# Kernel tuning notes

Measured on AMD Instinct MI355X. Metric: run time of the kernel, lower is better.

Reference implementation:

```python
import jax, jax.numpy as jnp
import numpy as np

N = 100000       # n_entities + n_users
E = 1000000      # edges
D = 64           # entity_dim (phase/mod half-width)
R = 40           # n_relations
PI = 3.1415926235897933
GAMMA = 12.0
EMB_RANGE = (GAMMA + 2.0) / D   # (gamma + epsilon) / entity_dim
DIMS = [128, 64, 32, 16]        # conv_dim_list = [2*D] + [64,32,16]


def setup_inputs() -> dict:
    key = jax.random.key(0)
    ks = jax.random.split(key, 20)
    inp = {}
    inp["entity_embed"] = jax.random.uniform(ks[0], (N, 2 * D), minval=-EMB_RANGE, maxval=EMB_RANGE, dtype=jnp.float32)
    inp["rel_embed"] = jax.random.uniform(ks[1], (R, 3 * D), minval=-EMB_RANGE, maxval=EMB_RANGE, dtype=jnp.float32)
    inp["phase_w"] = jnp.array([[0.5 * EMB_RANGE]], dtype=jnp.float32)
    inp["mod_w"] = jnp.array([[1.0]], dtype=jnp.float32)
    names = [("W1_0", "b1_0", "W2_0", "b2_0"), ("W1_1", "b1_1", "W2_1", "b2_1"), ("W1_2", "b1_2", "W1_2b", "b2_2")]
    for i, (w1n, b1n, w2n, b2n) in enumerate(names):
        din, dout = DIMS[i], DIMS[i + 1]
        s = 1.0 / np.sqrt(din)
        inp[w1n] = jax.random.uniform(ks[2 + 4 * i], (dout, din), minval=-s, maxval=s, dtype=jnp.float32)
        inp[b1n] = jax.random.uniform(ks[3 + 4 * i], (dout,), minval=-s, maxval=s, dtype=jnp.float32)
        inp[w2n] = jax.random.uniform(ks[4 + 4 * i], (dout, din), minval=-s, maxval=s, dtype=jnp.float32)
        inp[b2n] = jax.random.uniform(ks[5 + 4 * i], (dout,), minval=-s, maxval=s, dtype=jnp.float32)
    inp["src"] = jax.random.randint(ks[14], (E,), 0, N, dtype=jnp.int32)
    inp["dst"] = jax.random.randint(ks[15], (E,), 0, N, dtype=jnp.int32)
    inp["etype"] = jax.random.randint(ks[16], (E,), 0, R, dtype=jnp.int32)
    return inp


def _edge_att(entity_embed, rel_embed, phase_w, mod_w, src, dst, etype):
    # HAKE att_score: h = dst node, t = src node (per original code)
    h = entity_embed[dst]            # [E, 2D]
    t = entity_embed[src]            # [E, 2D]
    r = rel_embed[etype]             # [E, 3D]
    scale = EMB_RANGE / PI
    ph, mh = h[:, :D], h[:, D:]
    pr, mr, br = r[:, :D], r[:, D:2 * D], r[:, 2 * D:]
    pt, mt = t[:, :D], t[:, D:]
    mr = jnp.abs(mr)
    br = jnp.minimum(br, 1.0)
    br = jnp.where(br < -mr, -mr, br)  # conditional write bias_relation[indicator] = -mod_relation
    mod_score = jnp.linalg.norm(mh * (mr + br) - mt * (1.0 - br), axis=1) * mod_w[0, 0]
    phase = (ph + pr - pt) / scale
    phase_score = jnp.sum(jnp.abs(jnp.sin(phase / 2.0)), axis=1) * phase_w[0, 0]
    att = phase_score + mod_score    # [E]
    # edge softmax over incoming edges of each dst node
    amax = jax.ops.segment_max(att, dst, num_segments=N)
    ex = jnp.exp(att - amax[dst])
    den = jax.ops.segment_sum(ex, dst, num_segments=N)
    return ex / den[dst]


def reference(entity_embed, rel_embed, phase_w, mod_w,
              W1_0, b1_0, W2_0, b2_0,
              W1_1, b1_1, W2_1, b2_1,
              W1_2, b1_2, W1_2b, b2_2,
              src, dst, etype):
    att = _edge_att(entity_embed, rel_embed, phase_w, mod_w, src, dst, etype)

    def layer(node, W1, b1, W2, b2):
        # u_mul_e('node','att','side') + sum('side','N_h')
        msg = node[src] * att[:, None]                    # [E, din]
        Nh = jax.ops.segment_sum(msg, dst, num_segments=N)
        # bi-interaction aggregator
        o = jax.nn.leaky_relu((node + Nh) @ W1.T + b1) + jax.nn.leaky_relu((node * Nh) @ W2.T + b2)
        nrm = jnp.linalg.norm(o, axis=1, keepdims=True)
        return o, o / jnp.maximum(nrm, 1e-12)             # (ego_embed, F.normalize)

    ego = entity_embed
    outs = [ego]
    for (W1, b1, W2, b2) in [(W1_0, b1_0, W2_0, b2_0), (W1_1, b1_1, W2_1, b2_1), (W1_2, b1_2, W1_2b, b2_2)]:
        ego, normed = layer(ego, W1, b1, W2, b2)
        outs.append(normed)
    return jnp.concatenate(outs, axis=1)                   # [N, 128+64+32+16]
```

## Files before the change

kernel.cpp:

```cpp
#include <hip/hip_runtime.h>
#include <math.h>


__global__ void hist_kernel(const int* __restrict__ dst, int* __restrict__ cnt,
                            int nedges) {
    int e = blockIdx.x * blockDim.x + threadIdx.x;
    if (e < nedges) atomicAdd(&cnt[dst[e]], 1);
}

__global__ __launch_bounds__(1024) void scan_block_kernel(
    const int* __restrict__ cnt, int* __restrict__ rowptr,
    int* __restrict__ bsum, int n) {
    __shared__ int swv[16];
    int tid = threadIdx.x, lane = tid & 63, wid = tid >> 6;
    int i = blockIdx.x * 1024 + tid;
    int v = (i < n) ? cnt[i] : 0;
    #pragma unroll
    for (int off = 1; off < 64; off <<= 1) {
        int t = __shfl_up(v, off, 64);
        if (lane >= off) v += t;
    }
    if (lane == 63) swv[wid] = v;
    __syncthreads();
    if (wid == 0) {
        int s = (lane < 16) ? swv[lane] : 0;
        #pragma unroll
        for (int off = 1; off < 16; off <<= 1) {
            int t = __shfl_up(s, off, 64);
            if (lane >= off) s += t;
        }
        if (lane < 16) swv[lane] = s;
    }
    __syncthreads();
    int offv = wid ? swv[wid - 1] : 0;
    if (i < n) rowptr[i + 1] = v + offv;
    if (tid == 1023) bsum[blockIdx.x] = v + offv;
}

__global__ __launch_bounds__(64) void scan_tops_kernel(
    const int* __restrict__ bsum, int* __restrict__ boff, int nb) {
    int l = threadIdx.x;
    int a = (2 * l < nb) ? bsum[2 * l] : 0;
    int b = (2 * l + 1 < nb) ? bsum[2 * l + 1] : 0;
    int s = a + b;
    #pragma unroll
    for (int off = 1; off < 64; off <<= 1) {
        int t = __shfl_up(s, off, 64);
        if (l >= off) s += t;
    }
    int excl = s - (a + b);
    if (2 * l < nb) boff[2 * l] = excl;
    if (2 * l + 1 < nb) boff[2 * l + 1] = excl + a;
}

__global__ __launch_bounds__(1024) void scan_add_kernel(
    int* __restrict__ rowptr, const int* __restrict__ boff, int n) {
    int i = blockIdx.x * 1024 + threadIdx.x;
    if (i < n) rowptr[i + 1] += boff[blockIdx.x];
    if (i == 0) rowptr[0] = 0;
}

__global__ void fill_kernel(const int* __restrict__ src, const int* __restrict__ dst,
                            const int* __restrict__ etype,
                            const int* __restrict__ rowptr, int* __restrict__ cursor,
                            int* __restrict__ se_s, int nedges) {
    int e = blockIdx.x * blockDim.x + threadIdx.x;
    if (e >= nedges) return;
    int d = dst[e];
    int slot = rowptr[d] + atomicAdd(&cursor[d], 1);
    se_s[slot] = src[e] | (etype[e] << 17);
}

__global__ void rel_prep_kernel(const float* __restrict__ rel,
                                float* __restrict__ relp, int nrel) {
    int i = blockIdx.x * blockDim.x + threadIdx.x;
    if (i >= nrel * 64) return;
    int r = i >> 6, d = i & 63;
    float pr = rel[r * 192 + d];
    float mr = fabsf(rel[r * 192 + 64 + d]);
    float br = rel[r * 192 + 128 + d];
    br = fminf(br, 1.0f);
    br = fmaxf(br, -mr);
    relp[r * 192 + d]       = mr + br;
    relp[r * 192 + 64 + d]  = 1.0f - br;
    relp[r * 192 + 128 + d] = pr;
}

__global__ __launch_bounds__(256) void att_gather_kernel(
    const float* __restrict__ embed, const float* __restrict__ relp,
    const float* __restrict__ pw, const float* __restrict__ mw,
    const int* __restrict__ se_s, const int* __restrict__ rowptr,
    float* __restrict__ att_s, float* __restrict__ ai,
    float* __restrict__ Nh, int nnodes)
{
    int v = blockIdx.x * 4 + (threadIdx.x >> 6);
    if (v >= nnodes) return;
    int lane = threadIdx.x & 63;
    int sub = lane >> 5;
    int c = lane & 31;
    int beg = rowptr[v];
    int deg = rowptr[v + 1] - beg;

    const float K = (float)(0.5 * 3.1415926235897933 / 0.21875);
    float mwv = mw[0], pwv = pw[0];

    float4 h4 = *(const float4*)(embed + (size_t)v * 128 + 4 * c);

    float den = 0.0f;
    float4 acc = make_float4(0.f, 0.f, 0.f, 0.f);

    #pragma unroll 2
    for (int k0 = 0; k0 < deg; k0 += 2) {
        int ke = k0 + sub;
        bool valid = ke < deg;
        int kc = beg + (valid ? ke : 0);
        int se = se_s[kc];
        int sidx = se & 0x1FFFF;
        int r = se >> 17;
        float4 t4 = *(const float4*)(embed + (size_t)sidx * 128 + 4 * c);
        float rv;
        if (c < 16) {
            float4 P4 = *(const float4*)(relp + r * 192 + 128 + 4 * c);
            rv  = fabsf(__sinf((h4.x + P4.x - t4.x) * K));
            rv += fabsf(__sinf((h4.y + P4.y - t4.y) * K));
            rv += fabsf(__sinf((h4.z + P4.z - t4.z) * K));
            rv += fabsf(__sinf((h4.w + P4.w - t4.w) * K));
        } else {
            float4 A4 = *(const float4*)(relp + r * 192 + 4 * (c - 16));
            float4 B4 = *(const float4*)(relp + r * 192 + 64 + 4 * (c - 16));
            float d0 = h4.x * A4.x - t4.x * B4.x;
            float d1 = h4.y * A4.y - t4.y * B4.y;
            float d2 = h4.z * A4.z - t4.z * B4.z;
            float d3 = h4.w * A4.w - t4.w * B4.w;
            rv = (d0 * d0 + d1 * d1) + (d2 * d2 + d3 * d3);
        }
        #pragma unroll
        for (int off = 1; off < 16; off <<= 1)
            rv += __shfl_xor(rv, off, 64);
        float other = __shfl_xor(rv, 16, 64);
        float ppv = (c < 16) ? rv : other;
        float qqv = (c < 16) ? other : rv;
        float s = sqrtf(qqv) * mwv + ppv * pwv;
        float w = valid ? __expf(s) : 0.0f;
        den += w;
        acc.x = fmaf(w, t4.x, acc.x);
        acc.y = fmaf(w, t4.y, acc.y);
        acc.z = fmaf(w, t4.z, acc.z);
        acc.w = fmaf(w, t4.w, acc.w);
        if (valid && c == 0) att_s[kc] = w;
    }
    acc.x += __shfl_xor(acc.x, 32, 64);
    acc.y += __shfl_xor(acc.y, 32, 64);
    acc.z += __shfl_xor(acc.z, 32, 64);
    acc.w += __shfl_xor(acc.w, 32, 64);
    den += __shfl_xor(den, 32, 64);
    float invd = (deg > 0) ? 1.0f / den : 0.0f;
    if (sub == 0) {
        float4 o = make_float4(acc.x * invd, acc.y * invd,
                               acc.z * invd, acc.w * invd);
        *(float4*)(Nh + (size_t)v * 128 + 4 * c) = o;
        if (c == 0) ai[v] = invd;
    }
}

template<int DIN>
__global__ __launch_bounds__(256) void gather_kernel(
    const float* __restrict__ node, int nstride, const float* __restrict__ nrm,
    const float* __restrict__ att_s, const int* __restrict__ se_s,
    const int* __restrict__ rowptr, const float* __restrict__ ai,
    float* __restrict__ Nh, int nnodes)
{
    constexpr int LPE = DIN / 4;
    constexpr int EP  = 64 / LPE;
    constexpr int U   = 4;
    int v = blockIdx.x * 4 + (threadIdx.x >> 6);
    if (v >= nnodes) return;
    int lane = threadIdx.x & 63;
    int sub = lane / LPE;
    int c = lane % LPE;
    int beg = rowptr[v];
    int deg = rowptr[v + 1] - beg;

    float4 acc = make_float4(0.f, 0.f, 0.f, 0.f);
    for (int kb = 0; kb < deg; kb += 64) {
        int kc = kb + lane;
        bool inr = kc < deg;
        int sv = inr ? (se_s[beg + kc] & 0x1FFFF) : 0;
        float av = inr ? att_s[beg + kc] * nrm[sv] : 0.0f;
        int kmax = min(64, deg - kb);
        for (int k0 = 0; k0 < kmax; k0 += U * EP) {
            float a[U];
            const float4* p[U];
            #pragma unroll
            for (int u = 0; u < U; ++u) {
                int kk = k0 + u * EP + sub;
                bool val = kk < kmax;
                int kidx = val ? kk : 0;
                int ssrc = __shfl(sv, kidx, 64);
                float aa = __shfl(av, kidx, 64);
                a[u] = val ? aa : 0.0f;
                p[u] = (const float4*)(node + (size_t)ssrc * nstride + 4 * c);
            }
            float4 rv[U];
            #pragma unroll
            for (int u = 0; u < U; ++u) rv[u] = *p[u];
            #pragma unroll
            for (int u = 0; u < U; ++u) {
                acc.x += a[u] * rv[u].x;
                acc.y += a[u] * rv[u].y;
                acc.z += a[u] * rv[u].z;
                acc.w += a[u] * rv[u].w;
            }
        }
    }
    #pragma unroll
    for (int off = LPE; off < 64; off <<= 1) {
        acc.x += __shfl_xor(acc.x, off, 64);
        acc.y += __shfl_xor(acc.y, off, 64);
        acc.z += __shfl_xor(acc.z, off, 64);
        acc.w += __shfl_xor(acc.w, off, 64);
    }
    if (sub == 0) {
        float aiv = ai[v];
        float4 o = make_float4(acc.x * aiv, acc.y * aiv,
                               acc.z * aiv, acc.w * aiv);
        *(float4*)(Nh + (size_t)v * DIN + 4 * c) = o;
    }
}

template<int DIN, int DOUT, bool NRM>
__global__ __launch_bounds__(512) void gemm_kernel(
    const float* __restrict__ node, int nstride, const float* __restrict__ nrm_in,
    const float* __restrict__ Nh,
    const float* __restrict__ W1, const float* __restrict__ b1,
    const float* __restrict__ W2, const float* __restrict__ b2,
    float* __restrict__ out, int out_col, float* __restrict__ nrm_out, int nnodes)
{
    constexpr int XS = DIN + 1;
    constexpr int DH = DOUT / 8;
    __shared__ float sx1[64 * XS], sx2[64 * XS];
    __shared__ float sred[8][64];

    int tid = threadIdx.x;
    int tile0 = blockIdx.x * 64;

    for (int idx = tid; idx < 64 * (DIN / 4); idx += 512) {
        int row = idx / (DIN / 4), c = idx % (DIN / 4);
        int v = tile0 + row;
        float4 nv4 = make_float4(0.f, 0.f, 0.f, 0.f);
        float4 hv4 = make_float4(0.f, 0.f, 0.f, 0.f);
        if (v < nnodes) {
            nv4 = *(const float4*)(node + (size_t)v * nstride + 4 * c);
            hv4 = *(const float4*)(Nh + (size_t)v * DIN + 4 * c);
            if (NRM) {
                float rn = nrm_in[v];
                nv4.x *= rn; nv4.y *= rn; nv4.z *= rn; nv4.w *= rn;
            }
        }
        float* p1 = sx1 + row * XS + 4 * c;
        float* p2 = sx2 + row * XS + 4 * c;
        p1[0] = nv4.x + hv4.x; p1[1] = nv4.y + hv4.y;
        p1[2] = nv4.z + hv4.z; p1[3] = nv4.w + hv4.w;
        p2[0] = nv4.x * hv4.x; p2[1] = nv4.y * hv4.y;
        p2[2] = nv4.z * hv4.z; p2[3] = nv4.w * hv4.w;
    }
    __syncthreads();

    int lane = tid & 63;
    int jh = __builtin_amdgcn_readfirstlane(tid >> 6);
    int j0 = jh * DH;
    int v = tile0 + lane;
    bool act = v < nnodes;

    float acc1[DH], acc2[DH];
    #pragma unroll
    for (int j = 0; j < DH; ++j) { acc1[j] = 0.f; acc2[j] = 0.f; }

    const float* px1 = sx1 + lane * XS;
    const float* px2 = sx2 + lane * XS;
    #pragma unroll 1
    for (int ic = 0; ic < DIN; ic += 8) {
        float x1c[8], x2c[8];
        #pragma unroll
        for (int t = 0; t < 8; ++t) {
            x1c[t] = px1[ic + t];
            x2c[t] = px2[ic + t];
        }
        #pragma unroll
        for (int j = 0; j < DH; ++j) {
            const float* w1 = W1 + (size_t)(j0 + j) * DIN + ic;
            const float* w2 = W2 + (size_t)(j0 + j) * DIN + ic;
            #pragma unroll
            for (int t = 0; t < 8; ++t) {
                acc1[j] = fmaf(x1c[t], w1[t], acc1[j]);
                acc2[j] = fmaf(x2c[t], w2[t], acc2[j]);
            }
        }
    }

    float o[DH];
    float ss = 0.0f;
    #pragma unroll
    for (int j = 0; j < DH; ++j) {
        float a1 = acc1[j] + b1[j0 + j];
        a1 = a1 >= 0.0f ? a1 : 0.01f * a1;
        float a2 = acc2[j] + b2[j0 + j];
        a2 = a2 >= 0.0f ? a2 : 0.01f * a2;
        o[j] = a1 + a2;
        ss += o[j] * o[j];
    }
    sred[jh][lane] = ss;
    __syncthreads();
    float tot = 0.0f;
    #pragma unroll
    for (int q = 0; q < 8; ++q) tot += sred[q][lane];
    float nv2 = fmaxf(sqrtf(tot), 1e-12f);
    float inv = 1.0f / nv2;
    if (act) {
        float* po = out + (size_t)v * 240 + out_col + j0;
        if (DH >= 4) {
            #pragma unroll
            for (int j = 0; j < DH; j += 4) {
                float4 st = make_float4(o[j] * inv, o[j + 1] * inv,
                                        o[j + 2] * inv, o[j + 3] * inv);
                *(float4*)(po + j) = st;
            }
        } else {
            #pragma unroll
            for (int j = 0; j < DH; ++j) po[j] = o[j] * inv;
        }
        if (nrm_out && jh == 0) nrm_out[v] = nv2;
    }
}

__global__ void copy_ego_kernel(const float* __restrict__ embed,
                                float* __restrict__ out, int nnodes) {
    int tid = blockIdx.x * blockDim.x + threadIdx.x;
    if (tid >= nnodes * 32) return;
    int v = tid >> 5;
    int c = tid & 31;
    float4 val = *(const float4*)(embed + (size_t)v * 128 + 4 * c);
    *(float4*)(out + (size_t)v * 240 + 4 * c) = val;
}

extern "C" void kernel_launch(void* const* d_in, const int* in_sizes, int n_in,
                              void* d_out, int out_size, void* d_ws, size_t ws_size,
                              hipStream_t stream) {
    const float* embed = (const float*)d_in[0];
    const float* rel   = (const float*)d_in[1];
    const float* pw    = (const float*)d_in[2];
    const float* mw    = (const float*)d_in[3];
    const float* W1_0  = (const float*)d_in[4];
    const float* b1_0  = (const float*)d_in[5];
    const float* W2_0  = (const float*)d_in[6];
    const float* b2_0  = (const float*)d_in[7];
    const float* W1_1  = (const float*)d_in[8];
    const float* b1_1  = (const float*)d_in[9];
    const float* W2_1  = (const float*)d_in[10];
    const float* b2_1  = (const float*)d_in[11];
    const float* W1_2  = (const float*)d_in[12];
    const float* b1_2  = (const float*)d_in[13];
    const float* W1_2b = (const float*)d_in[14];
    const float* b2_2  = (const float*)d_in[15];
    const int* src   = (const int*)d_in[16];
    const int* dst   = (const int*)d_in[17];
    const int* etype = (const int*)d_in[18];
    float* out = (float*)d_out;

    const int n = in_sizes[0] / 128;
    const int e = in_sizes[16];
    const int r = in_sizes[1] / 192;

    char* ws = (char*)d_ws;
    float* att_s  = (float*)ws;
    int*   se_s   = (int*)(att_s + e);
    float* Nh     = (float*)(se_s + e);
    int*   rowptr = (int*)(Nh + (size_t)n * 128);
    int*   cnt    = rowptr + n + 1;
    int*   cursor = cnt + n;
    int*   bsum   = cursor + n;
    int*   boff   = bsum + 128;
    float* nrm1   = (float*)(boff + 128);
    float* nrm2   = nrm1 + n;
    float* relp   = nrm2 + n;
    float* ai     = relp + r * 192;

    const int NB = (n + 1023) / 1024;

    hipMemsetAsync(cnt, 0, (size_t)(2 * n) * 4, stream);
    hist_kernel<<<(e + 255) / 256, 256, 0, stream>>>(dst, cnt, e);
    scan_block_kernel<<<NB, 1024, 0, stream>>>(cnt, rowptr, bsum, n);
    scan_tops_kernel<<<1, 64, 0, stream>>>(bsum, boff, NB);
    scan_add_kernel<<<NB, 1024, 0, stream>>>(rowptr, boff, n);
    fill_kernel<<<(e + 255) / 256, 256, 0, stream>>>(src, dst, etype, rowptr,
                                                     cursor, se_s, e);
    rel_prep_kernel<<<(r * 64 + 255) / 256, 256, 0, stream>>>(rel, relp, r);

    int gblocks = (n + 3) / 4;
    int tiles = (n + 63) / 64;

    att_gather_kernel<<<gblocks, 256, 0, stream>>>(
        embed, relp, pw, mw, se_s, rowptr, att_s, ai, Nh, n);

    gemm_kernel<128, 64, false><<<tiles, 512, 0, stream>>>(
        embed, 128, nullptr, Nh, W1_0, b1_0, W2_0, b2_0, out, 128, nrm1, n);
    gather_kernel<64><<<gblocks, 256, 0, stream>>>(
        out + 128, 240, nrm1, att_s, se_s, rowptr, ai, Nh, n);
    gemm_kernel<64, 32, true><<<tiles, 512, 0, stream>>>(
        out + 128, 240, nrm1, Nh, W1_1, b1_1, W2_1, b2_1, out, 192, nrm2, n);
    gather_kernel<32><<<gblocks, 256, 0, stream>>>(
        out + 192, 240, nrm2, att_s, se_s, rowptr, ai, Nh, n);
    gemm_kernel<32, 16, true><<<tiles, 512, 0, stream>>>(
        out + 192, 240, nrm2, Nh, W1_2, b1_2, W1_2b, b2_2, out, 224, nullptr, n);

    copy_ego_kernel<<<(n * 32 + 255) / 256, 256, 0, stream>>>(embed, out, n);
}
```

Baseline: 517.8 us.

## Process eight edges per wavefront in attention gather and fuse ego copy into GEMM

The attention gather kernel now maps 8 lanes to each edge, each lane covering 8 phase and 8 modulus elements, so one wavefront handles 8 edges per iteration instead of 2. This cuts the shuffle-reduction depth per edge and improves memory-level parallelism for low-degree nodes, at the cost of more registers per lane and a longer final cross-group reduction. Separately, the first-layer GEMM writes the ego embedding into the output while it loads its tile, which removes the standalone copy kernel and its extra read of the embedding.

```diff
diff --git a/kernel.cpp b/kernel.cpp
--- a/kernel.cpp
+++ b/kernel.cpp
@@ -96,70 +96,110 @@
     int v = blockIdx.x * 4 + (threadIdx.x >> 6);
     if (v >= nnodes) return;
     int lane = threadIdx.x & 63;
-    int sub = lane >> 5;
-    int c = lane & 31;
+    int g = lane >> 3;
+    int q = lane & 7;
     int beg = rowptr[v];
     int deg = rowptr[v + 1] - beg;
 
     const float K = (float)(0.5 * 3.1415926235897933 / 0.21875);
     float mwv = mw[0], pwv = pw[0];
 
-    float4 h4 = *(const float4*)(embed + (size_t)v * 128 + 4 * c);
+    const float* hrow = embed + (size_t)v * 128;
+    float4 hp0 = *(const float4*)(hrow + 8 * q);
+    float4 hp1 = *(const float4*)(hrow + 8 * q + 4);
+    float4 hm0 = *(const float4*)(hrow + 64 + 8 * q);
+    float4 hm1 = *(const float4*)(hrow + 64 + 8 * q + 4);
 
     float den = 0.0f;
-    float4 acc = make_float4(0.f, 0.f, 0.f, 0.f);
-
-    #pragma unroll 2
-    for (int k0 = 0; k0 < deg; k0 += 2) {
-        int ke = k0 + sub;
+    float4 ap0 = make_float4(0.f, 0.f, 0.f, 0.f);
+    float4 ap1 = make_float4(0.f, 0.f, 0.f, 0.f);
+    float4 am0 = make_float4(0.f, 0.f, 0.f, 0.f);
+    float4 am1 = make_float4(0.f, 0.f, 0.f, 0.f);
+
+    for (int k0 = 0; k0 < deg; k0 += 8) {
+        int ke = k0 + g;
         bool valid = ke < deg;
         int kc = beg + (valid ? ke : 0);
         int se = se_s[kc];
         int sidx = se & 0x1FFFF;
         int r = se >> 17;
-        float4 t4 = *(const float4*)(embed + (size_t)sidx * 128 + 4 * c);
-        float rv;
-        if (c < 16) {
-            float4 P4 = *(const float4*)(relp + r * 192 + 128 + 4 * c);
-            rv  = fabsf(__sinf((h4.x + P4.x - t4.x) * K));
-            rv += fabsf(__sinf((h4.y + P4.y - t4.y) * K));
-            rv += fabsf(__sinf((h4.z + P4.z - t4.z) * K));
-            rv += fabsf(__sinf((h4.w + P4.w - t4.w) * K));
-        } else {
-            float4 A4 = *(const float4*)(relp + r * 192 + 4 * (c - 16));
-            float4 B4 = *(const float4*)(relp + r * 192 + 64 + 4 * (c - 16));
-            float d0 = h4.x * A4.x - t4.x * B4.x;
-            float d1 = h4.y * A4.y - t4.y * B4.y;
-            float d2 = h4.z * A4.z - t4.z * B4.z;
-            float d3 = h4.w * A4.w - t4.w * B4.w;
-            rv = (d0 * d0 + d1 * d1) + (d2 * d2 + d3 * d3);
-        }
+        const float* trow = embed + (size_t)sidx * 128;
+        float4 tp0 = *(const float4*)(trow + 8 * q);
+        float4 tp1 = *(const float4*)(trow + 8 * q + 4);
+        float4 tm0 = *(const float4*)(trow + 64 + 8 * q);
+        float4 tm1 = *(const float4*)(trow + 64 + 8 * q + 4);
+        const float* rrow = relp + r * 192;
+        float4 A0 = *(const float4*)(rrow + 8 * q);
+        float4 A1 = *(const float4*)(rrow + 8 * q + 4);
+        float4 B0 = *(const float4*)(rrow + 64 + 8 * q);
+        float4 B1 = *(const float4*)(rrow + 64 + 8 * q + 4);
+        float4 P0 = *(const float4*)(rrow + 128 + 8 * q);
+        float4 P1 = *(const float4*)(rrow + 128 + 8 * q + 4);
+
+        float pp;
+        pp  = fabsf(__sinf((hp0.x + P0.x - tp0.x) * K));
+        pp += fabsf(__sinf((hp0.y + P0.y - tp0.y) * K));
+        pp += fabsf(__sinf((hp0.z + P0.z - tp0.z) * K));
+        pp += fabsf(__sinf((hp0.w + P0.w - tp0.w) * K));
+        pp += fabsf(__sinf((hp1.x + P1.x - tp1.x) * K));
+        pp += fabsf(__sinf((hp1.y + P1.y - tp1.y) * K));
+        pp += fabsf(__sinf((hp1.z + P1.z - tp1.z) * K));
+        pp += fabsf(__sinf((hp1.w + P1.w - tp1.w) * K));
+
+        float d0 = hm0.x * A0.x - tm0.x * B0.x;
+        float d1 = hm0.y * A0.y - tm0.y * B0.y;
+        float d2 = hm0.z * A0.z - tm0.z * B0.z;
+        float d3 = hm0.w * A0.w - tm0.w * B0.w;
+        float d4 = hm1.x * A1.x - tm1.x * B1.x;
+        float d5 = hm1.y * A1.y - tm1.y * B1.y;
+        float d6 = hm1.z * A1.z - tm1.z * B1.z;
+        float d7 = hm1.w * A1.w - tm1.w * B1.w;
+        float qq = ((d0 * d0 + d1 * d1) + (d2 * d2 + d3 * d3)) +
+                   ((d4 * d4 + d5 * d5) + (d6 * d6 + d7 * d7));
+
         #pragma unroll
-        for (int off = 1; off < 16; off <<= 1)
-            rv += __shfl_xor(rv, off, 64);
-        float other = __shfl_xor(rv, 16, 64);
-        float ppv = (c < 16) ? rv : other;
-        float qqv = (c < 16) ? other : rv;
-        float s = sqrtf(qqv) * mwv + ppv * pwv;
+        for (int off = 1; off < 8; off <<= 1) {
+            pp += __shfl_xor(pp, off, 64);
+            qq += __shfl_xor(qq, off, 64);
+        }
+        float s = sqrtf(qq) * mwv + pp * pwv;
         float w = valid ? __expf(s) : 0.0f;
         den += w;
-        acc.x = fmaf(w, t4.x, acc.x);
-        acc.y = fmaf(w, t4.y, acc.y);
-        acc.z = fmaf(w, t4.z, acc.z);
-        acc.w = fmaf(w, t4.w, acc.w);
-        if (valid && c == 0) att_s[kc] = w;
-    }
-    acc.x += __shfl_xor(acc.x, 32, 64);
-    acc.y += __shfl_xor(acc.y, 32, 64);
-    acc.z += __shfl_xor(acc.z, 32, 64);
-    acc.w += __shfl_xor(acc.w, 32, 64);
-    den += __shfl_xor(den, 32, 64);
+        ap0.x = fmaf(w, tp0.x, ap0.x); ap0.y = fmaf(w, tp0.y, ap0.y);
+        ap0.z = fmaf(w, tp0.z, ap0.z); ap0.w = fmaf(w, tp0.w, ap0.w);
+        ap1.x = fmaf(w, tp1.x, ap1.x); ap1.y = fmaf(w, tp1.y, ap1.y);
+        ap1.z = fmaf(w, tp1.z, ap1.z); ap1.w = fmaf(w, tp1.w, ap1.w);
+        am0.x = fmaf(w, tm0.x, am0.x); am0.y = fmaf(w, tm0.y, am0.y);
+        am0.z = fmaf(w, tm0.z, am0.z); am0.w = fmaf(w, tm0.w, am0.w);
+        am1.x = fmaf(w, tm1.x, am1.x); am1.y = fmaf(w, tm1.y, am1.y);
+        am1.z = fmaf(w, tm1.z, am1.z); am1.w = fmaf(w, tm1.w, am1.w);
+        if (valid && q == 0) att_s[kc] = w;
+    }
+
+    #pragma unroll
+    for (int off = 8; off < 64; off <<= 1) {
+        ap0.x += __shfl_xor(ap0.x, off, 64); ap0.y += __shfl_xor(ap0.y, off, 64);
+        ap0.z += __shfl_xor(ap0.z, off, 64); ap0.w += __shfl_xor(ap0.w, off, 64);
+        ap1.x += __shfl_xor(ap1.x, off, 64); ap1.y += __shfl_xor(ap1.y, off, 64);
+        ap1.z += __shfl_xor(ap1.z, off, 64); ap1.w += __shfl_xor(ap1.w, off, 64);
+        am0.x += __shfl_xor(am0.x, off, 64); am0.y += __shfl_xor(am0.y, off, 64);
+        am0.z += __shfl_xor(am0.z, off, 64); am0.w += __shfl_xor(am0.w, off, 64);
+        am1.x += __shfl_xor(am1.x, off, 64); am1.y += __shfl_xor(am1.y, off, 64);
+        am1.z += __shfl_xor(am1.z, off, 64); am1.w += __shfl_xor(am1.w, off, 64);
+        den += __shfl_xor(den, off, 64);
+    }
     float invd = (deg > 0) ? 1.0f / den : 0.0f;
-    if (sub == 0) {
-        float4 o = make_float4(acc.x * invd, acc.y * invd,
-                               acc.z * invd, acc.w * invd);
-        *(float4*)(Nh + (size_t)v * 128 + 4 * c) = o;
-        if (c == 0) ai[v] = invd;
+    if (g == 0) {
+        float* pn = Nh + (size_t)v * 128;
+        *(float4*)(pn + 8 * q) = make_float4(ap0.x * invd, ap0.y * invd,
+                                             ap0.z * invd, ap0.w * invd);
+        *(float4*)(pn + 8 * q + 4) = make_float4(ap1.x * invd, ap1.y * invd,
+                                                 ap1.z * invd, ap1.w * invd);
+        *(float4*)(pn + 64 + 8 * q) = make_float4(am0.x * invd, am0.y * invd,
+                                                  am0.z * invd, am0.w * invd);
+        *(float4*)(pn + 64 + 8 * q + 4) = make_float4(am1.x * invd, am1.y * invd,
+                                                      am1.z * invd, am1.w * invd);
+        if (q == 0) ai[v] = invd;
     }
 }
 
@@ -228,7 +268,7 @@
     }
 }
 
-template<int DIN, int DOUT, bool NRM>
+template<int DIN, int DOUT, bool NRM, bool EGO>
 __global__ __launch_bounds__(512) void gemm_kernel(
     const float* __restrict__ node, int nstride, const float* __restrict__ nrm_in,
     const float* __restrict__ Nh,
@@ -252,6 +292,8 @@
         if (v < nnodes) {
             nv4 = *(const float4*)(node + (size_t)v * nstride + 4 * c);
             hv4 = *(const float4*)(Nh + (size_t)v * DIN + 4 * c);
+            if (EGO)
+                *(float4*)(out + (size_t)v * 240 + 4 * c) = nv4;
             if (NRM) {
                 float rn = nrm_in[v];
                 nv4.x *= rn; nv4.y *= rn; nv4.z *= rn; nv4.w *= rn;
@@ -331,16 +373,6 @@
         }
         if (nrm_out && jh == 0) nrm_out[v] = nv2;
     }
-}
-
-__global__ void copy_ego_kernel(const float* __restrict__ embed,
-                                float* __restrict__ out, int nnodes) {
-    int tid = blockIdx.x * blockDim.x + threadIdx.x;
-    if (tid >= nnodes * 32) return;
-    int v = tid >> 5;
-    int c = tid & 31;
-    float4 val = *(const float4*)(embed + (size_t)v * 128 + 4 * c);
-    *(float4*)(out + (size_t)v * 240 + 4 * c) = val;
 }
 
 extern "C" void kernel_launch(void* const* d_in, const int* in_sizes, int n_in,
@@ -402,16 +434,14 @@
     att_gather_kernel<<<gblocks, 256, 0, stream>>>(
         embed, relp, pw, mw, se_s, rowptr, att_s, ai, Nh, n);
 
-    gemm_kernel<128, 64, false><<<tiles, 512, 0, stream>>>(
+    gemm_kernel<128, 64, false, true><<<tiles, 512, 0, stream>>>(
         embed, 128, nullptr, Nh, W1_0, b1_0, W2_0, b2_0, out, 128, nrm1, n);
     gather_kernel<64><<<gblocks, 256, 0, stream>>>(
         out + 128, 240, nrm1, att_s, se_s, rowptr, ai, Nh, n);
-    gemm_kernel<64, 32, true><<<tiles, 512, 0, stream>>>(
+    gemm_kernel<64, 32, true, false><<<tiles, 512, 0, stream>>>(
         out + 128, 240, nrm1, Nh, W1_1, b1_1, W2_1, b2_1, out, 192, nrm2, n);
     gather_kernel<32><<<gblocks, 256, 0, stream>>>(
         out + 192, 240, nrm2, att_s, se_s, rowptr, ai, Nh, n);
-    gemm_kernel<32, 16, true><<<tiles, 512, 0, stream>>>(
+    gemm_kernel<32, 16, true, false><<<tiles, 512, 0, stream>>>(
         out + 192, 240, nrm2, Nh, W1_2, b1_2, W1_2b, b2_2, out, 224, nullptr, n);
-
-    copy_ego_kernel<<<(n * 32 + 255) / 256, 256, 0, stream>>>(embed, out, n);
-}
+}
```

Result: faster. 471.9 us (-8.9%).
